# Optimization experiments

Hardware: AMD Instinct MI355X
Metric: run time of the kernel (lower is better)

The kernel has to match this reference:

```python
import jax, jax.numpy as jnp
import numpy as np

NUM_HEADS = 16
BN_EPS = 1e-5


def setup_inputs() -> dict:
    key = jax.random.key(0)
    ks = jax.random.split(key, 12)
    B, S, D = 8, 1024, 1024
    s = 1.0 / np.sqrt(D)
    return {
        "key": jax.random.normal(ks[0], (B, S, D), jnp.float32),
        "value": jax.random.normal(ks[1], (B, S, D), jnp.float32),
        "query": jax.random.normal(ks[2], (B, S, D), jnp.float32),
        "Wk": jax.random.normal(ks[3], (D, D), jnp.float32) * s,
        "bk": jax.random.normal(ks[4], (D,), jnp.float32) * s,
        "Wv": jax.random.normal(ks[5], (D, D), jnp.float32) * s,
        "bv": jax.random.normal(ks[6], (D,), jnp.float32) * s,
        "Wq": jax.random.normal(ks[7], (D, D), jnp.float32) * s,
        "bq": jax.random.normal(ks[8], (D,), jnp.float32) * s,
        "Wf": jax.random.normal(ks[9], (D, D), jnp.float32) * s,
        "bf": jax.random.normal(ks[10], (D,), jnp.float32) * s,
        "gamma": jnp.ones((D,), jnp.float32),
        "beta": jnp.zeros((D,), jnp.float32),
    }


def _mha(key, value, query, Wk, bk, Wv, bv, Wq, bq, Wf, bf, gamma, beta):
    B, S, D = query.shape
    H = NUM_HEADS
    d = D // H
    residual = query

    k = key @ Wk + bk      # [B, S, D]
    v = value @ Wv + bv
    q = query @ Wq + bq

    # Faithful to torch: raw row-major view(B*H, -1, d) — NOT the standard head transpose.
    k = k.reshape(B * H, -1, d)   # [B*H, S, d]
    v = v.reshape(B * H, -1, d)
    q = q.reshape(B * H, -1, d)

    # Faithful quirky scale: (dim_per_head // num_heads) ** -0.5
    scale = jnp.float32((d // H) ** (-0.5))

    scores = jnp.einsum('bqd,bkd->bqk', q, k) * scale          # [B*H, S, S]
    attention = jax.nn.softmax(scores, axis=2)
    context = jnp.einsum('bqk,bkd->bqd', attention, v)          # [B*H, S, d]

    context = context.reshape(B, -1, D)                         # [B, S, D]
    out = context @ Wf + bf

    # BatchNorm1d over channel dim D (training mode: batch stats over B and S, biased var)
    x = residual + out                                          # [B, S, D]
    mean = jnp.mean(x, axis=(0, 1))
    var = jnp.mean((x - mean) ** 2, axis=(0, 1))
    out = (x - mean) * jax.lax.rsqrt(var + BN_EPS) * gamma + beta
    return out, attention


def reference(key, value, query, Wk, bk, Wv, bv, Wq, bq, Wf, bf, gamma, beta):
    return _mha(key, value, query, Wk, bk, Wv, bv, Wq, bq, Wf, bf, gamma, beta)
```

## Files before the change

kernel.cpp:

```cpp
#include <hip/hip_runtime.h>
#include <hip/hip_bf16.h>
#include <stdint.h>

typedef __attribute__((ext_vector_type(8))) short     short8;
typedef __attribute__((ext_vector_type(8))) _Float16  f16x8;
typedef __attribute__((ext_vector_type(4))) float     f32x4;
typedef __attribute__((ext_vector_type(4))) unsigned short ushort4_t;

__device__ inline unsigned short f2bf(float f) {
    unsigned u = __float_as_uint(f);
    u += 0x7fffu + ((u >> 16) & 1u);
    return (unsigned short)(u >> 16);
}
__device__ inline float bf2f(unsigned short h) {
    return __uint_as_float(((unsigned)h) << 16);
}
__device__ inline unsigned short f2h(float f) {
    _Float16 h = (_Float16)f;
    unsigned short r;
    __builtin_memcpy(&r, &h, 2);
    return r;
}

__device__ inline void gload16(const void* g, void* lds) {
    unsigned loff = (unsigned)(uintptr_t)lds;
    loff = __builtin_amdgcn_readfirstlane(loff);
    auto l = (__attribute__((address_space(3))) unsigned int*)(uintptr_t)loff;
    auto p = (const __attribute__((address_space(1))) unsigned int*)(uintptr_t)g;
    __builtin_amdgcn_global_load_lds(p, l, 16, 0, 0);
}

__global__ void cvt3_f32_2b(const float4* __restrict__ k, const float4* __restrict__ q,
                            const float4* __restrict__ v,
                            ushort4_t* __restrict__ k16, ushort4_t* __restrict__ q16,
                            ushort4_t* __restrict__ v16, int n4) {
    const int which = blockIdx.y;
    const float4* in  = which == 0 ? k   : which == 1 ? q   : v;
    ushort4_t*    out = which == 0 ? k16 : which == 1 ? q16 : v16;
    const bool tof16 = (which < 2);
    for (int i = blockIdx.x * blockDim.x + threadIdx.x; i < n4; i += gridDim.x * blockDim.x) {
        float4 vv = in[i];
        ushort4_t r;
        if (tof16) { r.x = f2h(vv.x);  r.y = f2h(vv.y);  r.z = f2h(vv.z);  r.w = f2h(vv.w); }
        else       { r.x = f2bf(vv.x); r.y = f2bf(vv.y); r.z = f2bf(vv.z); r.w = f2bf(vv.w); }
        out[i] = r;
    }
}

__global__ void transpose_cvt4(const float* __restrict__ Wk, const float* __restrict__ Wq,
                               const float* __restrict__ Wv, const float* __restrict__ Wf,
                               unsigned short* __restrict__ WkT, unsigned short* __restrict__ WqT,
                               unsigned short* __restrict__ WvT, unsigned short* __restrict__ WfT) {
    const int which = blockIdx.z;
    const float* W = which == 0 ? Wk : which == 1 ? Wq : which == 2 ? Wv : Wf;
    unsigned short* WT = which == 0 ? WkT : which == 1 ? WqT : which == 2 ? WvT : WfT;
    const bool tof16 = (which < 2);
    const int dim = 1024;

    __shared__ float t[32][33];
    const int bx = blockIdx.x * 32, by = blockIdx.y * 32;
    const int tx = threadIdx.x, ty = threadIdx.y;
#pragma unroll
    for (int i = 0; i < 4; ++i)
        t[ty + 8 * i][tx] = W[(size_t)(by + ty + 8 * i) * dim + bx + tx];
    __syncthreads();
#pragma unroll
    for (int i = 0; i < 4; ++i) {
        float v = t[tx][ty + 8 * i];
        WT[(size_t)(bx + ty + 8 * i) * dim + by + tx] = tof16 ? f2h(v) : f2bf(v);
    }
}

__global__ void transpose_v(const unsigned short* __restrict__ v, unsigned short* __restrict__ vT) {
    const int bh = blockIdx.z, d0 = blockIdx.x * 32, s0 = blockIdx.y * 32;
    __shared__ unsigned short t[32][33];
    const int tx = threadIdx.x, ty = threadIdx.y;
    const size_t base = (size_t)bh << 16;
#pragma unroll
    for (int i = 0; i < 4; ++i)
        t[ty + 8 * i][tx] = v[base + (size_t)(s0 + ty + 8 * i) * 64 + d0 + tx];
    __syncthreads();
#pragma unroll
    for (int i = 0; i < 4; ++i)
        vT[base + (size_t)(d0 + ty + 8 * i) * 1024 + s0 + tx] = t[tx][ty + 8 * i];
}

__global__ __launch_bounds__(256, 2) void qkv_gemm(
    const unsigned short* __restrict__ k16, const unsigned short* __restrict__ q16,
    const unsigned short* __restrict__ v16,
    const unsigned short* __restrict__ WkT, const unsigned short* __restrict__ WqT,
    const unsigned short* __restrict__ WvT,
    const float* __restrict__ bk, const float* __restrict__ bq, const float* __restrict__ bv,
    unsigned short* __restrict__ kout, unsigned short* __restrict__ qout,
    unsigned short* __restrict__ vout)
{
    const int which = blockIdx.y;
    const unsigned short* A   = which == 0 ? k16 : which == 1 ? q16 : v16;
    const unsigned short* Bt  = which == 0 ? WkT : which == 1 ? WqT : WvT;
    const float* bias         = which == 0 ? bk  : which == 1 ? bq  : bv;
    unsigned short* C2b       = which == 0 ? kout : which == 1 ? qout : vout;
    const bool f16in = (which < 2);
    const int N = 1024, K = 1024, nbx = 8;

    const int bid = blockIdx.x;
    const int cpx = gridDim.x >> 3;
    const int swz = (bid & 7) * cpx + (bid >> 3);
    const int bm = swz / nbx, bn = swz % nbx;
    const int m0 = bm * 128, n0 = bn * 128;

    const int tid = threadIdx.x;
    const int w = tid >> 6, l = tid & 63, g = l >> 4, c = l & 15;
    const int wr = w >> 1, wc = w & 1;

    __shared__ unsigned short As[2][8192];
    __shared__ unsigned short Bs[2][8192];

    f32x4 acc[4][4] = {};

    const int srow = tid >> 3, scol = (tid & 7) * 8;
    const unsigned short* ApS = A  + (size_t)(m0 + srow) * K + scol;
    const unsigned short* BpS = Bt + (size_t)(n0 + srow) * K + scol;

    const int NT = K >> 6;

#define STAGE_GEMM(bufi, koff)                                                \
    do {                                                                      \
        _Pragma("unroll")                                                     \
        for (int i = 0; i < 4; ++i) {                                         \
            gload16(ApS + (size_t)i * 32 * K + (koff), &As[bufi][(i * 256 + tid - l) * 8]); \
            gload16(BpS + (size_t)i * 32 * K + (koff), &Bs[bufi][(i * 256 + tid - l) * 8]); \
        }                                                                     \
    } while (0)

#define COMPUTE_GEMM(bufi)                                                         \
    do {                                                                           \
        _Pragma("unroll")                                                          \
        for (int kk = 0; kk < 2; ++kk) {                                           \
            if (f16in) {                                                           \
                f16x8 a[4], b[4];                                                  \
                _Pragma("unroll")                                                  \
                for (int mt = 0; mt < 4; ++mt)                                     \
                    a[mt] = *(const f16x8*)&As[bufi][(wr * 64 + mt * 16 + c) * 64 + kk * 32 + g * 8]; \
                _Pragma("unroll")                                                  \
                for (int nt = 0; nt < 4; ++nt)                                     \
                    b[nt] = *(const f16x8*)&Bs[bufi][(wc * 64 + nt * 16 + c) * 64 + kk * 32 + g * 8]; \
                _Pragma("unroll")                                                  \
                for (int mt = 0; mt < 4; ++mt)                                     \
                    _Pragma("unroll")                                              \
                    for (int nt = 0; nt < 4; ++nt)                                 \
                        acc[mt][nt] = __builtin_amdgcn_mfma_f32_16x16x32_f16(a[mt], b[nt], acc[mt][nt], 0, 0, 0); \
            } else {                                                               \
                short8 a[4], b[4];                                                 \
                _Pragma("unroll")                                                  \
                for (int mt = 0; mt < 4; ++mt)                                     \
                    a[mt] = *(const short8*)&As[bufi][(wr * 64 + mt * 16 + c) * 64 + kk * 32 + g * 8]; \
                _Pragma("unroll")                                                  \
                for (int nt = 0; nt < 4; ++nt)                                     \
                    b[nt] = *(const short8*)&Bs[bufi][(wc * 64 + nt * 16 + c) * 64 + kk * 32 + g * 8]; \
                _Pragma("unroll")                                                  \
                for (int mt = 0; mt < 4; ++mt)                                     \
                    _Pragma("unroll")                                              \
                    for (int nt = 0; nt < 4; ++nt)                                 \
                        acc[mt][nt] = __builtin_amdgcn_mfma_f32_16x16x32_bf16(a[mt], b[nt], acc[mt][nt], 0, 0, 0); \
            }                                                                      \
        }                                                                          \
    } while (0)

    STAGE_GEMM(0, 0);

#pragma unroll 2
    for (int kt = 0; kt < NT - 1; ++kt) {
        const int cur = kt & 1;
        STAGE_GEMM(cur ^ 1, (kt + 1) * 64);
        asm volatile("s_waitcnt vmcnt(8)" ::: "memory");
        __builtin_amdgcn_s_barrier();
        __builtin_amdgcn_sched_barrier(0);
        COMPUTE_GEMM(cur);
        __builtin_amdgcn_sched_barrier(0);
        __builtin_amdgcn_s_barrier();
    }
    asm volatile("s_waitcnt vmcnt(0)" ::: "memory");
    __builtin_amdgcn_s_barrier();
    __builtin_amdgcn_sched_barrier(0);
    COMPUTE_GEMM((NT - 1) & 1);

#undef STAGE_GEMM
#undef COMPUTE_GEMM

#pragma unroll
    for (int nt = 0; nt < 4; ++nt) {
        const int col = n0 + wc * 64 + nt * 16 + c;
        const float bs = bias[col];
#pragma unroll
        for (int mt = 0; mt < 4; ++mt) {
            const int row0 = m0 + wr * 64 + mt * 16 + g * 4;
#pragma unroll
            for (int r = 0; r < 4; ++r) {
                const float x = acc[mt][nt][r] + bs;
                const size_t idx = (size_t)(row0 + r) * N + col;
                C2b[idx] = f16in ? f2h(x) : f2bf(x);
            }
        }
    }
}

__global__ __launch_bounds__(256, 2) void gemm_out(
    const unsigned short* __restrict__ A,
    const unsigned short* __restrict__ Bt,
    const float* __restrict__ bias,
    const float* __restrict__ resid,
    float* __restrict__ Cf,
    float* __restrict__ psum,
    float* __restrict__ psq)
{
    const int N = 1024, K = 1024, nbx = 8;
    const int bid = blockIdx.x;
    const int cpx = gridDim.x >> 3;
    const int swz = (bid & 7) * cpx + (bid >> 3);
    const int bm = swz / nbx, bn = swz % nbx;
    const int m0 = bm * 128, n0 = bn * 128;

    const int tid = threadIdx.x;
    const int w = tid >> 6, l = tid & 63, g = l >> 4, c = l & 15;
    const int wr = w >> 1, wc = w & 1;

    __shared__ unsigned short As[2][8192];
    __shared__ unsigned short Bs[2][8192];
    __shared__ float sred[2][2][4][16][2];

    f32x4 acc[4][4] = {};

    const int srow = tid >> 3, scol = (tid & 7) * 8;
    const unsigned short* ApS = A  + (size_t)(m0 + srow) * K + scol;
    const unsigned short* BpS = Bt + (size_t)(n0 + srow) * K + scol;

    const int NT = K >> 6;

#define STAGE_GEMM(bufi, koff)                                                \
    do {                                                                      \
        _Pragma("unroll")                                                     \
        for (int i = 0; i < 4; ++i) {                                         \
            gload16(ApS + (size_t)i * 32 * K + (koff), &As[bufi][(i * 256 + tid - l) * 8]); \
            gload16(BpS + (size_t)i * 32 * K + (koff), &Bs[bufi][(i * 256 + tid - l) * 8]); \
        }                                                                     \
    } while (0)

#define COMPUTE_GEMM(bufi)                                                         \
    do {                                                                           \
        _Pragma("unroll")                                                          \
        for (int kk = 0; kk < 2; ++kk) {                                           \
            short8 a[4], b[4];                                                     \
            _Pragma("unroll")                                                      \
            for (int mt = 0; mt < 4; ++mt)                                         \
                a[mt] = *(const short8*)&As[bufi][(wr * 64 + mt * 16 + c) * 64 + kk * 32 + g * 8]; \
            _Pragma("unroll")                                                      \
            for (int nt = 0; nt < 4; ++nt)                                         \
                b[nt] = *(const short8*)&Bs[bufi][(wc * 64 + nt * 16 + c) * 64 + kk * 32 + g * 8]; \
            _Pragma("unroll")                                                      \
            for (int mt = 0; mt < 4; ++mt)                                         \
                _Pragma("unroll")                                                  \
                for (int nt = 0; nt < 4; ++nt)                                     \
                    acc[mt][nt] = __builtin_amdgcn_mfma_f32_16x16x32_bf16(a[mt], b[nt], acc[mt][nt], 0, 0, 0); \
        }                                                                          \
    } while (0)

    STAGE_GEMM(0, 0);

#pragma unroll 2
    for (int kt = 0; kt < NT - 1; ++kt) {
        const int cur = kt & 1;
        STAGE_GEMM(cur ^ 1, (kt + 1) * 64);
        asm volatile("s_waitcnt vmcnt(8)" ::: "memory");
        __builtin_amdgcn_s_barrier();
        __builtin_amdgcn_sched_barrier(0);
        COMPUTE_GEMM(cur);
        __builtin_amdgcn_sched_barrier(0);
        __builtin_amdgcn_s_barrier();
    }
    asm volatile("s_waitcnt vmcnt(0)" ::: "memory");
    __builtin_amdgcn_s_barrier();
    __builtin_amdgcn_sched_barrier(0);
    COMPUTE_GEMM((NT - 1) & 1);

#undef STAGE_GEMM
#undef COMPUTE_GEMM

    float s_nt[4] = {0.f, 0.f, 0.f, 0.f};
    float q_nt[4] = {0.f, 0.f, 0.f, 0.f};
#pragma unroll
    for (int nt = 0; nt < 4; ++nt) {
        const int col = n0 + wc * 64 + nt * 16 + c;
        const float bs = bias[col];
#pragma unroll
        for (int mt = 0; mt < 4; ++mt) {
            const int row0 = m0 + wr * 64 + mt * 16 + g * 4;
#pragma unroll
            for (int r = 0; r < 4; ++r) {
                const size_t idx = (size_t)(row0 + r) * N + col;
                const float xv = acc[mt][nt][r] + bs + resid[idx];
                Cf[idx] = xv;
                s_nt[nt] += xv;
                q_nt[nt] += xv * xv;
            }
        }
    }
#pragma unroll
    for (int nt = 0; nt < 4; ++nt) {
        s_nt[nt] += __shfl_xor(s_nt[nt], 16);
        s_nt[nt] += __shfl_xor(s_nt[nt], 32);
        q_nt[nt] += __shfl_xor(q_nt[nt], 16);
        q_nt[nt] += __shfl_xor(q_nt[nt], 32);
    }
    if (g == 0) {
#pragma unroll
        for (int nt = 0; nt < 4; ++nt) {
            sred[wr][wc][nt][c][0] = s_nt[nt];
            sred[wr][wc][nt][c][1] = q_nt[nt];
        }
    }
    __syncthreads();
    if (tid < 128) {
        const int wc2 = tid >> 6, nt2 = (tid >> 4) & 3, c2 = tid & 15;
        const float ss = sred[0][wc2][nt2][c2][0] + sred[1][wc2][nt2][c2][0];
        const float qq = sred[0][wc2][nt2][c2][1] + sred[1][wc2][nt2][c2][1];
        const int col = n0 + wc2 * 64 + nt2 * 16 + c2;
        psum[bm * 1024 + col] = ss;
        psq [bm * 1024 + col] = qq;
    }
}

__global__ __launch_bounds__(256, 4) void attn_kernel(
    const unsigned short* __restrict__ qf,
    const unsigned short* __restrict__ kf,
    const unsigned short* __restrict__ vT,
    float* __restrict__ attn_out,
    unsigned short* __restrict__ ctx)
{
    const int L = blockIdx.x;
    const int rb = (L >> 3) & 63;
    const int bh = ((L & 7) << 4) | (L >> 9);

    const int tid = threadIdx.x;
    const int w = tid >> 6, l = tid & 63, g = l >> 4, c = l & 15;
    const int n0 = w * 256;

    __shared__ unsigned short P[16 * 1024];
    __shared__ float rs_lds[4][16];
    __shared__ float inv_lds[16];

    const unsigned short* qb = qf + ((size_t)bh << 16) + (size_t)(rb * 16 + c) * 64 + g * 8;
    const f16x8 q0 = *(const f16x8*)(qb);
    const f16x8 q1 = *(const f16x8*)(qb + 32);

    const unsigned short* kb = kf + ((size_t)bh << 16);
    const unsigned swzc = ((unsigned)(c & 7)) << 4;
    const unsigned prow = (unsigned)c * 2048;

    ushort4_t pks[16];
    float rsum = 0.f;

#pragma unroll
    for (int t = 0; t < 16; ++t) {
        const unsigned short* kp = kb + (size_t)(n0 + t * 16 + c) * 64 + g * 8;
        const f16x8 a0 = *(const f16x8*)(kp);
        const f16x8 a1 = *(const f16x8*)(kp + 32);
        f32x4 s = {0.f, 0.f, 0.f, 0.f};
        s = __builtin_amdgcn_mfma_f32_16x16x32_f16(a0, q0, s, 0, 0, 0);
        s = __builtin_amdgcn_mfma_f32_16x16x32_f16(a1, q1, s, 0, 0, 0);

        const float p0 = __expf(s[0] * 0.5f);
        const float p1 = __expf(s[1] * 0.5f);
        const float p2 = __expf(s[2] * 0.5f);
        const float p3 = __expf(s[3] * 0.5f);
        rsum += (p0 + p1) + (p2 + p3);

        ushort4_t pk;
        pk.x = f2bf(p0); pk.y = f2bf(p1); pk.z = f2bf(p2); pk.w = f2bf(p3);
        pks[t] = pk;
        *(ushort4_t*)((char*)P + ((prow + (unsigned)(n0 * 2 + t * 32 + g * 8)) ^ swzc)) = pk;
    }

    rsum += __shfl_xor(rsum, 16);
    rsum += __shfl_xor(rsum, 32);
    if (g == 0) rs_lds[w][c] = rsum;
    __syncthreads();
    if (tid < 16)
        inv_lds[tid] = 1.0f / (rs_lds[0][tid] + rs_lds[1][tid] + rs_lds[2][tid] + rs_lds[3][tid]);
    __syncthreads();

    const int rA = l >> 3, jj = l & 7;
    const int rB = 8 + rA;
    const int slA = ((jj & 3) << 4) | rA;
    const int slB = ((jj & 3) << 4) | rB;
    const float invA = inv_lds[rA];
    const float invB = inv_lds[rB];
    float* aoA = attn_out + ((size_t)bh << 20) + (size_t)(rb * 16 + rA) * 1024 + n0;
    float* aoB = attn_out + ((size_t)bh << 20) + (size_t)(rb * 16 + rB) * 1024 + n0;

    f32x4 pacc = {0.f, 0.f, 0.f, 0.f};
    const unsigned short* vb = vT + ((size_t)bh << 16) + (size_t)(w * 16 + c) * 1024;
#pragma unroll
    for (int ks = 0; ks < 32; ++ks) {
        const short8 a = *(const short8*)((char*)P + ((prow + (unsigned)(ks * 64 + g * 16)) ^ swzc));
        const short8 b = *(const short8*)(vb + ks * 32 + g * 8);
        pacc = __builtin_amdgcn_mfma_f32_16x16x32_bf16(a, b, pacc, 0, 0, 0);
        if (ks & 1) {
            const int p = ks >> 2;
            const int t0 = 2 * p, t1 = t0 + 1;
            const bool isA = ((ks & 3) == 1);
            const int sl = isA ? slA : slB;
            unsigned long long e0, e1;
            __builtin_memcpy(&e0, &pks[t0], 8);
            __builtin_memcpy(&e1, &pks[t1], 8);
            const unsigned long long ea = __shfl(e0, sl, 64);
            const unsigned long long eb = __shfl(e1, sl, 64);
            const unsigned long long sel = (jj < 4) ? ea : eb;
            const float inv2 = isA ? invA : invB;
            f32x4 o;
            o[0] = bf2f((unsigned short)(sel      )) * inv2;
            o[1] = bf2f((unsigned short)(sel >> 16)) * inv2;
            o[2] = bf2f((unsigned short)(sel >> 32)) * inv2;
            o[3] = bf2f((unsigned short)(sel >> 48)) * inv2;
            float* dst = (isA ? aoA : aoB) + p * 32 + jj * 4;
            __builtin_nontemporal_store(o, (f32x4*)dst);
        }
    }
    unsigned short* cb = ctx + ((size_t)bh << 16) + (size_t)(rb * 16) * 64 + w * 16 + c;
#pragma unroll
    for (int r = 0; r < 4; ++r) {
        const int row = g * 4 + r;
        cb[(size_t)row * 64] = f2bf(pacc[r] * inv_lds[row]);
    }
}

__global__ void bn_final(const float* __restrict__ psum, const float* __restrict__ psq,
                         const float* __restrict__ gamma, const float* __restrict__ beta,
                         float* __restrict__ ab) {
    const int cidx = threadIdx.x;
    float s = 0.f, q = 0.f;
#pragma unroll 8
    for (int i = 0; i < 64; ++i) { s += psum[i * 1024 + cidx]; q += psq[i * 1024 + cidx]; }
    const float mean = s * (1.0f / 8192.0f);
    const float var  = q * (1.0f / 8192.0f) - mean * mean;
    const float a = gamma[cidx] * rsqrtf(var + 1e-5f);
    ab[cidx]        = a;
    ab[1024 + cidx] = beta[cidx] - mean * a;
}

__global__ void bn_apply(const float4* __restrict__ x4, const float* __restrict__ ab, float4* __restrict__ o4) {
    const int n4 = 2 * 1024 * 1024;
    for (int i = blockIdx.x * blockDim.x + threadIdx.x; i < n4; i += gridDim.x * blockDim.x) {
        const float4 v = x4[i];
        const int c0 = (i & 255) << 2;
        float4 r;
        r.x = v.x * ab[c0 + 0] + ab[1024 + c0 + 0];
        r.y = v.y * ab[c0 + 1] + ab[1024 + c0 + 1];
        r.z = v.z * ab[c0 + 2] + ab[1024 + c0 + 2];
        r.w = v.w * ab[c0 + 3] + ab[1024 + c0 + 3];
        o4[i] = r;
    }
}

extern "C" void kernel_launch(void* const* d_in, const int* in_sizes, int n_in,
                              void* d_out, int out_size, void* d_ws, size_t ws_size,
                              hipStream_t stream) {
    (void)in_sizes; (void)n_in; (void)out_size; (void)ws_size;

    const float* key   = (const float*)d_in[0];
    const float* value = (const float*)d_in[1];
    const float* query = (const float*)d_in[2];
    const float* Wk = (const float*)d_in[3];
    const float* bk = (const float*)d_in[4];
    const float* Wv = (const float*)d_in[5];
    const float* bv = (const float*)d_in[6];
    const float* Wq = (const float*)d_in[7];
    const float* bq = (const float*)d_in[8];
    const float* Wf = (const float*)d_in[9];
    const float* bff = (const float*)d_in[10];
    const float* gamma = (const float*)d_in[11];
    const float* beta  = (const float*)d_in[12];

    char* ws = (char*)d_ws;
    const size_t MB = 1u << 20;
    unsigned short* key16   = (unsigned short*)(ws + 0);
    unsigned short* ctx     = (unsigned short*)(ws + 0);
    unsigned short* query16 = (unsigned short*)(ws + 16 * MB);
    unsigned short* value16 = (unsigned short*)(ws + 32 * MB);
    float*          xbuf    = (float*)(ws + 16 * MB);
    unsigned short* WkT = (unsigned short*)(ws + 48 * MB);
    unsigned short* WqT = (unsigned short*)(ws + 50 * MB);
    unsigned short* WvT = (unsigned short*)(ws + 52 * MB);
    unsigned short* WfT = (unsigned short*)(ws + 54 * MB);
    unsigned short* kbuf = (unsigned short*)(ws + 56 * MB);
    unsigned short* qbuf = (unsigned short*)(ws + 72 * MB);
    unsigned short* vbuf = (unsigned short*)(ws + 88 * MB);
    float* psum = (float*)(ws + 88 * MB);
    float* psq  = (float*)(ws + 88 * MB + 256 * 1024);
    float* ab   = (float*)(ws + 88 * MB + 512 * 1024);
    unsigned short* vTbuf = (unsigned short*)(ws + 104 * MB);

    float* out0 = (float*)d_out;
    float* attn = out0 + 8388608;

    const int n4big = 2 * 1024 * 1024;

    cvt3_f32_2b<<<dim3(1024, 3), 256, 0, stream>>>(
        (const float4*)key, (const float4*)query, (const float4*)value,
        (ushort4_t*)key16, (ushort4_t*)query16, (ushort4_t*)value16, n4big);

    dim3 tb(32, 8);
    transpose_cvt4<<<dim3(32, 32, 4), tb, 0, stream>>>(Wk, Wq, Wv, Wf, WkT, WqT, WvT, WfT);

    qkv_gemm<<<dim3(512, 3), 256, 0, stream>>>(
        key16, query16, value16, WkT, WqT, WvT, bk, bq, bv, kbuf, qbuf, vbuf);

    transpose_v<<<dim3(2, 32, 128), tb, 0, stream>>>(vbuf, vTbuf);

    attn_kernel<<<8192, 256, 0, stream>>>(qbuf, kbuf, vTbuf, attn, ctx);

    gemm_out<<<512, 256, 0, stream>>>(ctx, WfT, bff, query, xbuf, psum, psq);

    bn_final<<<1, 1024, 0, stream>>>(psum, psq, gamma, beta, ab);
    bn_apply<<<2048, 256, 0, stream>>>((const float4*)xbuf, ab, (float4*)out0);
}
```

Baseline: 403.3 us.

## Halve attention query-row tile to 8 rows per block for higher occupancy

```diff
diff --git a/kernel.cpp b/kernel.cpp
--- a/kernel.cpp
+++ b/kernel.cpp
@@ -329,7 +329,7 @@
     }
 }
 
-__global__ __launch_bounds__(256, 4) void attn_kernel(
+__global__ __launch_bounds__(256, 6) void attn_kernel(
     const unsigned short* __restrict__ qf,
     const unsigned short* __restrict__ kf,
     const unsigned short* __restrict__ vT,
@@ -337,24 +337,25 @@
     unsigned short* __restrict__ ctx)
 {
     const int L = blockIdx.x;
-    const int rb = (L >> 3) & 63;
-    const int bh = ((L & 7) << 4) | (L >> 9);
+    const int rb = (L >> 3) & 127;
+    const int bh = ((L & 7) << 4) | (L >> 10);
 
     const int tid = threadIdx.x;
     const int w = tid >> 6, l = tid & 63, g = l >> 4, c = l & 15;
+    const int cr = c & 7;
     const int n0 = w * 256;
 
-    __shared__ unsigned short P[16 * 1024];
-    __shared__ float rs_lds[4][16];
-    __shared__ float inv_lds[16];
-
-    const unsigned short* qb = qf + ((size_t)bh << 16) + (size_t)(rb * 16 + c) * 64 + g * 8;
+    __shared__ unsigned short P[8 * 1024];
+    __shared__ float rs_lds[4][8];
+    __shared__ float inv_lds[8];
+
+    const unsigned short* qb = qf + ((size_t)bh << 16) + (size_t)(rb * 8 + cr) * 64 + g * 8;
     const f16x8 q0 = *(const f16x8*)(qb);
     const f16x8 q1 = *(const f16x8*)(qb + 32);
 
     const unsigned short* kb = kf + ((size_t)bh << 16);
-    const unsigned swzc = ((unsigned)(c & 7)) << 4;
-    const unsigned prow = (unsigned)c * 2048;
+    const unsigned swzc = ((unsigned)cr) << 4;
+    const unsigned prow = (unsigned)cr * 2048;
 
     ushort4_t pks[16];
     float rsum = 0.f;
@@ -377,25 +378,22 @@
         ushort4_t pk;
         pk.x = f2bf(p0); pk.y = f2bf(p1); pk.z = f2bf(p2); pk.w = f2bf(p3);
         pks[t] = pk;
-        *(ushort4_t*)((char*)P + ((prow + (unsigned)(n0 * 2 + t * 32 + g * 8)) ^ swzc)) = pk;
+        if (c < 8)
+            *(ushort4_t*)((char*)P + ((prow + (unsigned)(n0 * 2 + t * 32 + g * 8)) ^ swzc)) = pk;
     }
 
     rsum += __shfl_xor(rsum, 16);
     rsum += __shfl_xor(rsum, 32);
-    if (g == 0) rs_lds[w][c] = rsum;
+    if (g == 0 && c < 8) rs_lds[w][c] = rsum;
     __syncthreads();
-    if (tid < 16)
+    if (tid < 8)
         inv_lds[tid] = 1.0f / (rs_lds[0][tid] + rs_lds[1][tid] + rs_lds[2][tid] + rs_lds[3][tid]);
     __syncthreads();
 
-    const int rA = l >> 3, jj = l & 7;
-    const int rB = 8 + rA;
-    const int slA = ((jj & 3) << 4) | rA;
-    const int slB = ((jj & 3) << 4) | rB;
-    const float invA = inv_lds[rA];
-    const float invB = inv_lds[rB];
-    float* aoA = attn_out + ((size_t)bh << 20) + (size_t)(rb * 16 + rA) * 1024 + n0;
-    float* aoB = attn_out + ((size_t)bh << 20) + (size_t)(rb * 16 + rB) * 1024 + n0;
+    const int r8 = l >> 3, jj = l & 7;
+    const int sl = ((jj & 3) << 4) | r8;
+    const float invS = inv_lds[r8];
+    float* aoS = attn_out + ((size_t)bh << 20) + (size_t)(rb * 8 + r8) * 1024 + n0;
 
     f32x4 pacc = {0.f, 0.f, 0.f, 0.f};
     const unsigned short* vb = vT + ((size_t)bh << 16) + (size_t)(w * 16 + c) * 1024;
@@ -404,32 +402,30 @@
         const short8 a = *(const short8*)((char*)P + ((prow + (unsigned)(ks * 64 + g * 16)) ^ swzc));
         const short8 b = *(const short8*)(vb + ks * 32 + g * 8);
         pacc = __builtin_amdgcn_mfma_f32_16x16x32_bf16(a, b, pacc, 0, 0, 0);
-        if (ks & 1) {
+        if ((ks & 3) == 3) {
             const int p = ks >> 2;
             const int t0 = 2 * p, t1 = t0 + 1;
-            const bool isA = ((ks & 3) == 1);
-            const int sl = isA ? slA : slB;
             unsigned long long e0, e1;
             __builtin_memcpy(&e0, &pks[t0], 8);
             __builtin_memcpy(&e1, &pks[t1], 8);
             const unsigned long long ea = __shfl(e0, sl, 64);
             const unsigned long long eb = __shfl(e1, sl, 64);
             const unsigned long long sel = (jj < 4) ? ea : eb;
-            const float inv2 = isA ? invA : invB;
             f32x4 o;
-            o[0] = bf2f((unsigned short)(sel      )) * inv2;
-            o[1] = bf2f((unsigned short)(sel >> 16)) * inv2;
-            o[2] = bf2f((unsigned short)(sel >> 32)) * inv2;
-            o[3] = bf2f((unsigned short)(sel >> 48)) * inv2;
-            float* dst = (isA ? aoA : aoB) + p * 32 + jj * 4;
-            __builtin_nontemporal_store(o, (f32x4*)dst);
+            o[0] = bf2f((unsigned short)(sel      )) * invS;
+            o[1] = bf2f((unsigned short)(sel >> 16)) * invS;
+            o[2] = bf2f((unsigned short)(sel >> 32)) * invS;
+            o[3] = bf2f((unsigned short)(sel >> 48)) * invS;
+            __builtin_nontemporal_store(o, (f32x4*)(aoS + p * 32 + jj * 4));
         }
     }
-    unsigned short* cb = ctx + ((size_t)bh << 16) + (size_t)(rb * 16) * 64 + w * 16 + c;
-#pragma unroll
-    for (int r = 0; r < 4; ++r) {
-        const int row = g * 4 + r;
-        cb[(size_t)row * 64] = f2bf(pacc[r] * inv_lds[row]);
+    if (g < 2) {
+        unsigned short* cb = ctx + ((size_t)bh << 16) + (size_t)(rb * 8) * 64 + w * 16 + c;
+#pragma unroll
+        for (int r = 0; r < 4; ++r) {
+            const int row = g * 4 + r;
+            cb[(size_t)row * 64] = f2bf(pacc[r] * inv_lds[row]);
+        }
     }
 }
 
@@ -516,7 +512,7 @@
 
     transpose_v<<<dim3(2, 32, 128), tb, 0, stream>>>(vbuf, vTbuf);
 
-    attn_kernel<<<8192, 256, 0, stream>>>(qbuf, kbuf, vTbuf, attn, ctx);
+    attn_kernel<<<16384, 256, 0, stream>>>(qbuf, kbuf, vTbuf, attn, ctx);
 
     gemm_out<<<512, 256, 0, stream>>>(ctx, WfT, bff, query, xbuf, psum, psq);
 
```

Result: slower. 727.6 us (+80.4%).
